# Kernel tuning notes

Hardware: AMD Instinct MI355X
Metric: run time of the kernel (lower is better)

Reference implementation:

```python
import jax, jax.numpy as jnp
import numpy as np

HEAD_DIM = 64
NUM_LANDMARKS = 64
SEQ_LEN = 4096
N_ITER = 6


def setup_inputs() -> dict:
    key = jax.random.key(0)
    kq, kk, kv = jax.random.split(key, 3)
    shape = (4, 12, SEQ_LEN, HEAD_DIM)  # [B, H, S, D]
    return {
        "Q": jax.random.normal(kq, shape, dtype=jnp.float32),
        "K": jax.random.normal(kk, shape, dtype=jnp.float32),
        "V": jax.random.normal(kv, shape, dtype=jnp.float32),
    }


def iterative_inv(mat, n_iter=N_ITER):
    # Newton-Schulz iteration for Moore-Penrose pseudo-inverse.
    L = mat.shape[-1]
    I = jnp.eye(L, dtype=mat.dtype)
    Km = mat
    # global (over all batch/head) max of row/col L1 norms
    scale = 1.0 / (jnp.max(jnp.sum(jnp.abs(Km), axis=-2)) * jnp.max(jnp.sum(jnp.abs(Km), axis=-1)))
    Vm = scale * jnp.swapaxes(Km, -1, -2)
    for _ in range(n_iter):
        KV = jnp.matmul(Km, Vm)
        Vm = jnp.matmul(0.25 * Vm, 13.0 * I - jnp.matmul(KV, 15.0 * I - jnp.matmul(KV, 7.0 * I - KV)))
    return Vm


def reference(Q, K, V):
    B, H, S, D = Q.shape
    m = NUM_LANDMARKS
    inv_scale = 1.0 / np.sqrt(np.sqrt(HEAD_DIM))
    Q = Q * inv_scale
    K = K * inv_scale
    # landmark pooling: mean over segments of length S // m
    Q_land = Q.reshape(B, H, m, S // m, D).mean(axis=-2)  # [B,H,m,D]
    K_land = K.reshape(B, H, m, S // m, D).mean(axis=-2)  # [B,H,m,D]
    kernel_1 = jax.nn.softmax(jnp.einsum("bhsd,bhmd->bhsm", Q, K_land), axis=-1)      # [B,H,S,m]
    kernel_2 = jax.nn.softmax(jnp.einsum("bhmd,bhnd->bhmn", Q_land, K_land), axis=-1)  # [B,H,m,m]
    kernel_3 = jax.nn.softmax(jnp.einsum("bhmd,bhsd->bhms", Q_land, K), axis=-1)       # [B,H,m,S]
    X = jnp.matmul(jnp.matmul(kernel_1, iterative_inv(kernel_2)), jnp.matmul(kernel_3, V))
    return X
```

## Files before the change

### kernel.cpp

```cpp
#include <hip/hip_runtime.h>
#include <cstdint>

#define BH 48
#define SEQ 4096
#define DIM 64
#define SEG 64
#define NCHUNK 8
#define CHUNK 512
#define PAD 68
#define BSTR 72

static constexpr float INV_SCALE = 0.35355339059327379f;

#define OFF_QL   0u
#define OFF_KL   196608u
#define OFF_K2   393216u
#define OFF_W    589824u
#define OFF_P    786432u
#define OFF_MNUM 983040u
#define OFF_MDEN 2555904u
#define OFF_CMAX 2580480u
#define OFF_RMAX 2580528u

typedef __attribute__((ext_vector_type(8))) short short8;
typedef __attribute__((ext_vector_type(4))) float f32x4;
#define MFMA16(a,b,c) __builtin_amdgcn_mfma_f32_16x16x32_bf16(a,b,c,0,0,0)

__device__ __forceinline__ float4 ld4(const float* p){ return *reinterpret_cast<const float4*>(p); }
__device__ __forceinline__ void st4(float* p, float4 v){ *reinterpret_cast<float4*>(p) = v; }

__device__ __forceinline__ unsigned short bfh_(float x){
  unsigned u = __float_as_uint(x);
  return (unsigned short)((u + 0x7fffu + ((u>>16)&1u)) >> 16);
}
__device__ __forceinline__ unsigned short bfl_(float x, unsigned short h){
  float r = x - __uint_as_float(((unsigned)h)<<16);
  return (unsigned short)(__float_as_uint(r) >> 16);
}
__device__ __forceinline__ void split4(float4 v, uint2& hi, uint2& lo){
  unsigned short h0=bfh_(v.x), h1=bfh_(v.y), h2=bfh_(v.z), h3=bfh_(v.w);
  unsigned short l0=bfl_(v.x,h0), l1=bfl_(v.y,h1), l2=bfl_(v.z,h2), l3=bfl_(v.w,h3);
  hi = make_uint2((unsigned)h0 | ((unsigned)h1<<16), (unsigned)h2 | ((unsigned)h3<<16));
  lo = make_uint2((unsigned)l0 | ((unsigned)l1<<16), (unsigned)l2 | ((unsigned)l3<<16));
}
__device__ __forceinline__ short8 mk8(uint2 a, uint2 b){
  union { short8 s; uint4 u; } x; x.u = make_uint4(a.x,a.y,b.x,b.y); return x.s;
}

__device__ __forceinline__ void mm_tile(float c[4][4], const float (*A)[PAD], const float (*B)[PAD], int i0, int j0){
  #pragma unroll 4
  for(int k=0;k<64;k+=4){
    float4 a4[4];
    #pragma unroll
    for(int r=0;r<4;r++) a4[r] = ld4(&A[i0+r][k]);
    #pragma unroll
    for(int kk=0;kk<4;kk++){
      float4 bv = ld4(&B[k+kk][j0]);
      #pragma unroll
      for(int r=0;r<4;r++){
        float a = ((const float*)&a4[r])[kk];
        c[r][0] += a*bv.x; c[r][1] += a*bv.y; c[r][2] += a*bv.z; c[r][3] += a*bv.w;
      }
    }
  }
}

__device__ __forceinline__ void mm_tile_gA(float c[4][4], const float* __restrict__ gA, const float (*B)[PAD], int i0, int j0){
  #pragma unroll 4
  for(int k=0;k<64;k+=4){
    float4 a4[4];
    #pragma unroll
    for(int r=0;r<4;r++) a4[r] = ld4(gA + (i0+r)*64 + k);
    #pragma unroll
    for(int kk=0;kk<4;kk++){
      float4 bv = ld4(&B[k+kk][j0]);
      #pragma unroll
      for(int r=0;r<4;r++){
        float a = ((const float*)&a4[r])[kk];
        c[r][0] += a*bv.x; c[r][1] += a*bv.y; c[r][2] += a*bv.z; c[r][3] += a*bv.w;
      }
    }
  }
}

__device__ __forceinline__ void mm_tile_diag(float c[4][4], const float (*A)[PAD], const float (*B)[PAD], int i0, int j0, float dg){
  #pragma unroll 4
  for(int k=0;k<64;k+=4){
    float4 a4[4];
    #pragma unroll
    for(int r=0;r<4;r++) a4[r] = ld4(&A[i0+r][k]);
    #pragma unroll
    for(int kk=0;kk<4;kk++){
      float4 bv = ld4(&B[k+kk][j0]);
      float b0=-bv.x, b1=-bv.y, b2=-bv.z, b3=-bv.w;
      int dd = k+kk-j0;
      if(dd==0) b0+=dg; else if(dd==1) b1+=dg; else if(dd==2) b2+=dg; else if(dd==3) b3+=dg;
      #pragma unroll
      for(int r=0;r<4;r++){
        float a = ((const float*)&a4[r])[kk];
        c[r][0]+=a*b0; c[r][1]+=a*b1; c[r][2]+=a*b2; c[r][3]+=a*b3;
      }
    }
  }
}

__global__ __launch_bounds__(256) void pool_kernel(const float* __restrict__ Qg, const float* __restrict__ Kg, float* __restrict__ ws){
  int bx = blockIdx.x;
  int head = bx >> 5;
  int rest = bx & 31;
  int tensor = rest >> 4;
  int l0 = (rest & 15) * 4;
  int t = threadIdx.x;
  int ll = t >> 6;
  int lane = t & 63;
  int d4 = (lane & 15) * 4;
  int rq = lane >> 4;
  const float* src = tensor ? Kg : Qg;
  float* dst = ws + (tensor ? OFF_KL : OFF_QL);
  int l = l0 + ll;
  const float* base = src + ((size_t)head*SEQ + (size_t)l*SEG)*DIM + d4;
  float sx=0.f, sy=0.f, sz=0.f, sw=0.f;
  #pragma unroll 4
  for(int r=rq; r<SEG; r+=4){
    float4 v = ld4(base + (size_t)r*DIM);
    sx+=v.x; sy+=v.y; sz+=v.z; sw+=v.w;
  }
  sx += __shfl_xor(sx,16); sy += __shfl_xor(sy,16); sz += __shfl_xor(sz,16); sw += __shfl_xor(sw,16);
  sx += __shfl_xor(sx,32); sy += __shfl_xor(sy,32); sz += __shfl_xor(sz,32); sw += __shfl_xor(sw,32);
  if(rq==0){
    const float sc = INV_SCALE / 64.0f;
    float4 o; o.x=sx*sc; o.y=sy*sc; o.z=sz*sc; o.w=sw*sc;
    st4(dst + ((size_t)head*64 + l)*DIM + d4, o);
  }
}

__global__ __launch_bounds__(256) void k2_kernel(float* __restrict__ ws){
  __shared__ float sQ[64][65];
  __shared__ float sK[64][65];
  __shared__ float sE[64][65];
  __shared__ float red[128];
  int h = blockIdx.x, t = threadIdx.x;
  const float* QL = ws + OFF_QL + (size_t)h*4096;
  const float* KL = ws + OFF_KL + (size_t)h*4096;
  for(int i=t;i<4096;i+=256){ sQ[i>>6][i&63]=QL[i]; sK[i>>6][i&63]=KL[i]; }
  __syncthreads();
  int i = t>>2, q = t&3;
  float l[16];
  #pragma unroll
  for(int jj=0;jj<16;jj++){
    int j = q*16+jj;
    float s=0.f;
    for(int d=0;d<64;d++) s += sQ[i][d]*sK[j][d];
    l[jj]=s;
  }
  float mx = l[0];
  #pragma unroll
  for(int jj=1;jj<16;jj++) mx = fmaxf(mx,l[jj]);
  mx = fmaxf(mx, __shfl_xor(mx,1));
  mx = fmaxf(mx, __shfl_xor(mx,2));
  float sum=0.f;
  #pragma unroll
  for(int jj=0;jj<16;jj++){ l[jj]=__expf(l[jj]-mx); sum+=l[jj]; }
  sum += __shfl_xor(sum,1);
  sum += __shfl_xor(sum,2);
  float inv = 1.0f/sum;
  #pragma unroll
  for(int jj=0;jj<16;jj++) sE[i][q*16+jj] = l[jj]*inv;
  __syncthreads();
  float* K2 = ws + OFF_K2 + (size_t)h*4096;
  for(int idx=t; idx<4096; idx+=256) K2[idx] = sE[idx>>6][idx&63];
  if(t<64){
    float cs=0.f, rs=0.f;
    for(int r=0;r<64;r++){ cs += sE[r][t]; rs += sE[t][r]; }
    red[t]=cs; red[64+t]=rs;
  }
  __syncthreads();
  if(t==0){
    float cm=0.f, rm=0.f;
    for(int j=0;j<64;j++){ cm=fmaxf(cm,red[j]); rm=fmaxf(rm,red[64+j]); }
    ws[OFF_CMAX+h]=cm; ws[OFF_RMAX+h]=rm;
  }
}

__global__ __launch_bounds__(256) void fused_kernel(const float* __restrict__ Kg, const float* __restrict__ Vg, float* __restrict__ ws){
  __shared__ __align__(16) unsigned char smem[74752];
  __shared__ float sscale;
  int bid = blockIdx.x, t = threadIdx.x;
  const int lane=t&63, w=t>>6, ln=lane&15, g=lane>>4;
  const int rr=t>>4, c4=(t&15)*4;
  if(bid < BH){
    int h = bid;
    const float* K2 = ws + OFF_K2 + (size_t)h*4096;
    unsigned short* Uh=(unsigned short*)smem;
    unsigned short* Ul=Uh+4608;
    unsigned short* Rh=Uh+9216;
    unsigned short* Rl=Uh+13824;
    unsigned short* Ch=Uh+18432;
    unsigned short* Cl=Uh+23040;
    unsigned short* Gh=Uh+27648;
    unsigned short* Gl=Uh+32256;
    short8 kmh[2],kml[2];
    #pragma unroll
    for(int kh=0;kh<2;kh++){
      const float* p=K2+(16*w+ln)*64+32*kh+8*g;
      float4 x0=ld4(p), x1=ld4(p+4);
      uint2 h0,l0,h1,l1; split4(x0,h0,l0); split4(x1,h1,l1);
      kmh[kh]=mk8(h0,h1); kml[kh]=mk8(l0,l1);
    }
    if(t<64){
      float cm=(lane<BH)?ws[OFF_CMAX+lane]:0.f;
      float rm=(lane<BH)?ws[OFF_RMAX+lane]:0.f;
      #pragma unroll
      for(int s=32;s>=1;s>>=1){ cm=fmaxf(cm,__shfl_xor(cm,s)); rm=fmaxf(rm,__shfl_xor(rm,s)); }
      if(t==0) sscale=1.0f/(cm*rm);
    }
    __syncthreads();
    float scale=sscale;
    #pragma unroll
    for(int gg=0;gg<4;gg++){
      int m=rr+16*gg;
      float4 v=ld4(K2+m*64+c4);
      v.x*=scale; v.y*=scale; v.z*=scale; v.w*=scale;
      uint2 hi,lo; split4(v,hi,lo);
      *reinterpret_cast<uint2*>(Uh+m*BSTR+c4)=hi;
      *reinterpret_cast<uint2*>(Ul+m*BSTR+c4)=lo;
      float fv[4]={v.x,v.y,v.z,v.w};
      #pragma unroll
      for(int e=0;e<4;e++){
        unsigned short hv=bfh_(fv[e]);
        Rh[(c4+e)*BSTR+m]=hv;
        Rl[(c4+e)*BSTR+m]=bfl_(fv[e],hv);
      }
    }
    __syncthreads();
    f32x4 dA[4];
    short8 ah[2],al[2];
    for(int it=0; it<5; it++){
      #pragma unroll
      for(int ni=0;ni<4;ni++){
        f32x4 d=(f32x4){0.f,0.f,0.f,0.f};
        #pragma unroll
        for(int kh=0;kh<2;kh++){
          int bb=(16*ni+ln)*BSTR+32*kh+8*g;
          short8 bh=*reinterpret_cast<const short8*>(Uh+bb);
          short8 bl=*reinterpret_cast<const short8*>(Ul+bb);
          d=MFMA16(kmh[kh],bh,d); d=MFMA16(kmh[kh],bl,d); d=MFMA16(kml[kh],bh,d);
        }
        dA[ni]=d;
      }
      #pragma unroll
      for(int ni=0;ni<4;ni++){
        int j=16*ni+ln;
        float4 tv; float* pv=(float*)&tv;
        #pragma unroll
        for(int r=0;r<4;r++){
          float v=dA[ni][r];
          int i=16*w+4*g+r;
          unsigned short hv=bfh_(v);
          Ch[i*BSTR+j]=hv; Cl[i*BSTR+j]=bfl_(v,hv);
          pv[r]=((i==j)?7.0f:0.0f)-v;
        }
        uint2 hi,lo; split4(tv,hi,lo);
        *reinterpret_cast<uint2*>(Gh+j*BSTR+16*w+4*g)=hi;
        *reinterpret_cast<uint2*>(Gl+j*BSTR+16*w+4*g)=lo;
      }
      __syncthreads();
      #pragma unroll
      for(int kh=0;kh<2;kh++){
        int ab=(16*w+ln)*BSTR+32*kh+8*g;
        ah[kh]=*reinterpret_cast<const short8*>(Ch+ab);
        al[kh]=*reinterpret_cast<const short8*>(Cl+ab);
      }
      #pragma unroll
      for(int ni=0;ni<4;ni++){
        f32x4 d=(f32x4){0.f,0.f,0.f,0.f};
        #pragma unroll
        for(int kh=0;kh<2;kh++){
          int bb=(16*ni+ln)*BSTR+32*kh+8*g;
          short8 bh=*reinterpret_cast<const short8*>(Gh+bb);
          short8 bl=*reinterpret_cast<const short8*>(Gl+bb);
          d=MFMA16(ah[kh],bh,d); d=MFMA16(ah[kh],bl,d); d=MFMA16(al[kh],bh,d);
        }
        dA[ni]=d;
      }
      __syncthreads();
      #pragma unroll
      for(int ni=0;ni<4;ni++){
        int j=16*ni+ln;
        float4 tv; float* pv=(float*)&tv;
        #pragma unroll
        for(int r=0;r<4;r++){ int i=16*w+4*g+r; pv[r]=((i==j)?15.0f:0.0f)-dA[ni][r]; }
        uint2 hi,lo; split4(tv,hi,lo);
        *reinterpret_cast<uint2*>(Gh+j*BSTR+16*w+4*g)=hi;
        *reinterpret_cast<uint2*>(Gl+j*BSTR+16*w+4*g)=lo;
      }
      __syncthreads();
      #pragma unroll
      for(int ni=0;ni<4;ni++){
        f32x4 d=(f32x4){0.f,0.f,0.f,0.f};
        #pragma unroll
        for(int kh=0;kh<2;kh++){
          int bb=(16*ni+ln)*BSTR+32*kh+8*g;
          short8 bh=*reinterpret_cast<const short8*>(Gh+bb);
          short8 bl=*reinterpret_cast<const short8*>(Gl+bb);
          d=MFMA16(ah[kh],bh,d); d=MFMA16(ah[kh],bl,d); d=MFMA16(al[kh],bh,d);
        }
        dA[ni]=d;
      }
      __syncthreads();
      #pragma unroll
      for(int ni=0;ni<4;ni++){
        int j=16*ni+ln;
        float4 tv; float* pv=(float*)&tv;
        #pragma unroll
        for(int r=0;r<4;r++){ int i=16*w+4*g+r; pv[r]=((i==j)?13.0f:0.0f)-dA[ni][r]; }
        uint2 hi,lo; split4(tv,hi,lo);
        *reinterpret_cast<uint2*>(Ch+j*BSTR+16*w+4*g)=hi;
        *reinterpret_cast<uint2*>(Cl+j*BSTR+16*w+4*g)=lo;
      }
      __syncthreads();
      #pragma unroll
      for(int kh=0;kh<2;kh++){
        int ab=(16*w+ln)*BSTR+32*kh+8*g;
        ah[kh]=*reinterpret_cast<const short8*>(Rh+ab);
        al[kh]=*reinterpret_cast<const short8*>(Rl+ab);
      }
      #pragma unroll
      for(int ni=0;ni<4;ni++){
        f32x4 d=(f32x4){0.f,0.f,0.f,0.f};
        #pragma unroll
        for(int kh=0;kh<2;kh++){
          int bb=(16*ni+ln)*BSTR+32*kh+8*g;
          short8 bh=*reinterpret_cast<const short8*>(Ch+bb);
          short8 bl=*reinterpret_cast<const short8*>(Cl+bb);
          d=MFMA16(ah[kh],bh,d); d=MFMA16(ah[kh],bl,d); d=MFMA16(al[kh],bh,d);
        }
        dA[ni]=d;
      }
      __syncthreads();
      #pragma unroll
      for(int ni=0;ni<4;ni++){
        int j=16*ni+ln;
        float4 tv; float* pv=(float*)&tv;
        #pragma unroll
        for(int r=0;r<4;r++){
          float v=0.25f*dA[ni][r];
          int i=16*w+4*g+r;
          unsigned short hv=bfh_(v);
          Rh[i*BSTR+j]=hv; Rl[i*BSTR+j]=bfl_(v,hv);
          pv[r]=v;
        }
        uint2 hi,lo; split4(tv,hi,lo);
        *reinterpret_cast<uint2*>(Uh+j*BSTR+16*w+4*g)=hi;
        *reinterpret_cast<uint2*>(Ul+j*BSTR+16*w+4*g)=lo;
      }
      __syncthreads();
    }
    float (*Vmf)[PAD]=(float(*)[PAD])(smem+36864);
    for(int i=t;i<4096;i+=256){
      int r_=i>>6, c_=i&63;
      float v=__uint_as_float(((unsigned)Rh[r_*BSTR+c_])<<16)
             +__uint_as_float(((unsigned)Rl[r_*BSTR+c_])<<16);
      Vmf[r_][c_]=v;
    }
    __syncthreads();
    float (*B1)[PAD]=(float(*)[PAD])(smem);
    float (*B2)[PAD]=(float(*)[PAD])(smem+17408);
    int i0=(t>>4)*4, j0=(t&15)*4;
    {
      float c[4][4]={};
      mm_tile_gA(c,K2,Vmf,i0,j0);
      #pragma unroll
      for(int r=0;r<4;r++){ float4 o; o.x=c[r][0];o.y=c[r][1];o.z=c[r][2];o.w=c[r][3]; st4(&B1[i0+r][j0],o); }
      __syncthreads();
    }
    {
      float c[4][4]={};
      mm_tile_diag(c,B1,B1,i0,j0,7.0f);
      #pragma unroll
      for(int r=0;r<4;r++){ float4 o; o.x=c[r][0];o.y=c[r][1];o.z=c[r][2];o.w=c[r][3]; st4(&B2[i0+r][j0],o); }
      __syncthreads();
    }
    {
      float c[4][4]={};
      mm_tile_diag(c,B1,B2,i0,j0,15.0f);
      __syncthreads();
      #pragma unroll
      for(int r=0;r<4;r++){ float4 o; o.x=c[r][0];o.y=c[r][1];o.z=c[r][2];o.w=c[r][3]; st4(&B1[i0+r][j0],o); }
      __syncthreads();
    }
    {
      float c[4][4]={};
      mm_tile_diag(c,Vmf,B1,i0,j0,13.0f);
      __syncthreads();
      #pragma unroll
      for(int r=0;r<4;r++){ float4 o; o.x=0.25f*c[r][0];o.y=0.25f*c[r][1];o.z=0.25f*c[r][2];o.w=0.25f*c[r][3]; st4(&Vmf[i0+r][j0],o); }
      __syncthreads();
    }
    float* W = ws + OFF_W + (size_t)h*4096;
    for(int i=t;i<4096;i+=256) W[i] = Vmf[i>>6][i&63];
  } else {
    int b = bid - BH;
    int h = b >> 3, ch = b & 7;
    unsigned short* QLh=(unsigned short*)smem;
    unsigned short* QLl=QLh+4608;
    unsigned short* Kth=QLh+9216;
    unsigned short* Ktl=QLh+13824;
    unsigned short* VTh=QLh+18432;
    unsigned short* VTl=QLh+23040;
    unsigned short* PTh=QLh+27648;
    unsigned short* PTl=QLh+32256;
    float* sden=(float*)(smem+73728);
    const float* QL = ws + OFF_QL + (size_t)h*4096;
    #pragma unroll
    for(int gg=0;gg<4;gg++){
      int m=rr+16*gg;
      float4 v=ld4(QL+m*64+c4);
      uint2 hi,lo; split4(v,hi,lo);
      *reinterpret_cast<uint2*>(QLh+m*BSTR+c4)=hi;
      *reinterpret_cast<uint2*>(QLl+m*BSTR+c4)=lo;
    }
    const size_t kbase=((size_t)h*SEQ+(size_t)ch*CHUNK)*DIM;
    float4 kr[4],vr[4];
    #pragma unroll
    for(int gg=0;gg<4;gg++){
      size_t off=kbase+(size_t)(rr+16*gg)*DIM+c4;
      kr[gg]=ld4(Kg+off); vr[gg]=ld4(Vg+off);
    }
    f32x4 acc[4];
    #pragma unroll
    for(int ni=0;ni<4;ni++) acc[ni]=(f32x4){0.f,0.f,0.f,0.f};
    float den_acc[4]={0.f,0.f,0.f,0.f};
    for(int tile=0;tile<8;tile++){
      __syncthreads();
      #pragma unroll
      for(int gg=0;gg<4;gg++){
        int r=rr+16*gg;
        float4 kv=kr[gg];
        kv.x*=INV_SCALE; kv.y*=INV_SCALE; kv.z*=INV_SCALE; kv.w*=INV_SCALE;
        uint2 hi,lo; split4(kv,hi,lo);
        *reinterpret_cast<uint2*>(Kth+r*BSTR+c4)=hi;
        *reinterpret_cast<uint2*>(Ktl+r*BSTR+c4)=lo;
        float fv[4]={vr[gg].x,vr[gg].y,vr[gg].z,vr[gg].w};
        #pragma unroll
        for(int e=0;e<4;e++){
          int d=c4+e;
          unsigned short hv=bfh_(fv[e]);
          unsigned short lv=bfl_(fv[e],hv);
          int sp = r ^ (((d>>2)&7)<<3);
          VTh[d*BSTR+sp]=hv; VTl[d*BSTR+sp]=lv;
        }
      }
      if(tile<7){
        #pragma unroll
        for(int gg=0;gg<4;gg++){
          size_t off=kbase+(size_t)((tile+1)*64+rr+16*gg)*DIM+c4;
          kr[gg]=ld4(Kg+off); vr[gg]=ld4(Vg+off);
        }
      }
      __syncthreads();
      short8 kah[2],kal[2];
      #pragma unroll
      for(int kh=0;kh<2;kh++){
        int ab=(16*w+ln)*BSTR+32*kh+8*g;
        kah[kh]=*reinterpret_cast<const short8*>(Kth+ab);
        kal[kh]=*reinterpret_cast<const short8*>(Ktl+ab);
      }
      #pragma unroll
      for(int ni=0;ni<4;ni++){
        f32x4 dl=(f32x4){0.f,0.f,0.f,0.f};
        #pragma unroll
        for(int kh=0;kh<2;kh++){
          int bb=(16*ni+ln)*BSTR+32*kh+8*g;
          short8 bh=*reinterpret_cast<const short8*>(QLh+bb);
          short8 bl=*reinterpret_cast<const short8*>(QLl+bb);
          dl=MFMA16(kah[kh],bh,dl);
          dl=MFMA16(kah[kh],bl,dl);
          dl=MFMA16(kal[kh],bh,dl);
        }
        float p0=__expf(dl[0]), p1=__expf(dl[1]), p2=__expf(dl[2]), p3=__expf(dl[3]);
        den_acc[ni]+=p0+p1+p2+p3;
        unsigned short h0=bfh_(p0),h1=bfh_(p1),h2=bfh_(p2),h3=bfh_(p3);
        unsigned short l0=bfl_(p0,h0),l1=bfl_(p1,h1),l2=bfl_(p2,h2),l3=bfl_(p3,h3);
        int pb=(16*ni+ln)*BSTR+16*w+4*g;
        *reinterpret_cast<uint2*>(PTh+pb)=make_uint2((unsigned)h0|((unsigned)h1<<16),(unsigned)h2|((unsigned)h3<<16));
        *reinterpret_cast<uint2*>(PTl+pb)=make_uint2((unsigned)l0|((unsigned)l1<<16),(unsigned)l2|((unsigned)l3<<16));
      }
      __syncthreads();
      short8 pah[2],pal[2];
      #pragma unroll
      for(int kh=0;kh<2;kh++){
        int pb=(16*w+ln)*BSTR+32*kh+8*g;
        pah[kh]=*reinterpret_cast<const short8*>(PTh+pb);
        pal[kh]=*reinterpret_cast<const short8*>(PTl+pb);
      }
      #pragma unroll
      for(int ni=0;ni<4;ni++){
        int row=16*ni+ln;
        int swz=((row>>2)&7)<<3;
        #pragma unroll
        for(int kh=0;kh<2;kh++){
          int vb=row*BSTR+((32*kh+8*g)^swz);
          short8 vh=*reinterpret_cast<const short8*>(VTh+vb);
          short8 vl=*reinterpret_cast<const short8*>(VTl+vb);
          acc[ni]=MFMA16(pah[kh],vh,acc[ni]);
          acc[ni]=MFMA16(pah[kh],vl,acc[ni]);
          acc[ni]=MFMA16(pal[kh],vh,acc[ni]);
        }
      }
    }
    float* num = ws + OFF_MNUM + (size_t)b*4096;
    #pragma unroll
    for(int ni=0;ni<4;ni++){
      #pragma unroll
      for(int r=0;r<4;r++) num[(16*w+4*g+r)*64+16*ni+ln]=acc[ni][r];
      den_acc[ni]+=__shfl_xor(den_acc[ni],16);
      den_acc[ni]+=__shfl_xor(den_acc[ni],32);
    }
    if(lane<16){
      #pragma unroll
      for(int ni=0;ni<4;ni++) sden[w*64+16*ni+lane]=den_acc[ni];
    }
    __syncthreads();
    if(t<64) ws[OFF_MDEN+(size_t)b*64+t]=sden[t]+sden[64+t]+sden[128+t]+sden[192+t];
  }
}

__global__ __launch_bounds__(256) void combine_kernel(float* __restrict__ ws){
  __shared__ float sW[64][PAD];
  __shared__ float sM[64][PAD];
  __shared__ float sden[64];
  int h=blockIdx.x, t=threadIdx.x;
  if(t<64){
    float s=0.f;
    for(int c=0;c<NCHUNK;c++) s += ws[OFF_MDEN + ((size_t)h*NCHUNK+c)*64 + t];
    sden[t]=1.0f/s;
  }
  for(int i=t;i<4096;i+=256) sW[i>>6][i&63] = ws[OFF_W + (size_t)h*4096 + i];
  __syncthreads();
  for(int i=t;i<1024;i+=256){
    int m=i>>4, d4=(i&15)*4;
    float sx=0.f,sy=0.f,sz=0.f,sw2=0.f;
    for(int c=0;c<NCHUNK;c++){
      float4 v = ld4(ws + OFF_MNUM + ((size_t)h*NCHUNK+c)*4096 + m*64 + d4);
      sx+=v.x; sy+=v.y; sz+=v.z; sw2+=v.w;
    }
    float iv = sden[m];
    float4 o; o.x=sx*iv; o.y=sy*iv; o.z=sz*iv; o.w=sw2*iv;
    st4(&sM[m][d4], o);
  }
  __syncthreads();
  int i0=(t>>4)*4, j0=(t&15)*4;
  float c[4][4]={};
  mm_tile(c, sW, sM, i0, j0);
  float* P = ws + OFF_P + (size_t)h*4096;
  #pragma unroll
  for(int r=0;r<4;r++){
    float4 o; o.x=c[r][0]; o.y=c[r][1]; o.z=c[r][2]; o.w=c[r][3];
    st4(P + (i0+r)*64 + j0, o);
  }
}

__global__ __launch_bounds__(256) void final_kernel(const float* __restrict__ Qg, float* __restrict__ out, const float* __restrict__ ws){
  __shared__ __align__(16) unsigned char smem[37888];
  int bid=blockIdx.x, t=threadIdx.x;
  int h=bid>>6, s0=(bid&63)*64;
  const int lane=t&63, w=t>>6, ln=lane&15, g=lane>>4;
  const int rr=t>>4, c4=(t&15)*4;
  unsigned short* QBh=(unsigned short*)smem;
  unsigned short* QBl=QBh+4608;
  unsigned short* KLh=QBh+9216;
  unsigned short* KLl=QBh+13824;
  float* sdenw=(float*)(smem+36864);
  const float* KL = ws + OFF_KL + (size_t)h*4096;
  const float* P  = ws + OFF_P  + (size_t)h*4096;
  const float* Qb = Qg + ((size_t)h*SEQ + (size_t)s0)*DIM;
  float4 p2r[4];
  #pragma unroll
  for(int gg=0;gg<4;gg++){
    int row=rr+16*gg;
    p2r[gg]=ld4(P+row*64+c4);
    float4 q=ld4(Qb+(size_t)row*DIM+c4);
    q.x*=INV_SCALE; q.y*=INV_SCALE; q.z*=INV_SCALE; q.w*=INV_SCALE;
    uint2 hi,lo; split4(q,hi,lo);
    *reinterpret_cast<uint2*>(QBh+row*BSTR+c4)=hi;
    *reinterpret_cast<uint2*>(QBl+row*BSTR+c4)=lo;
    float4 kl=ld4(KL+row*64+c4);
    split4(kl,hi,lo);
    *reinterpret_cast<uint2*>(KLh+row*BSTR+c4)=hi;
    *reinterpret_cast<uint2*>(KLl+row*BSTR+c4)=lo;
  }
  __syncthreads();
  short8 ah_[2],al_[2];
  #pragma unroll
  for(int kh=0;kh<2;kh++){
    int ab=(16*w+ln)*BSTR+32*kh+8*g;
    ah_[kh]=*reinterpret_cast<const short8*>(KLh+ab);
    al_[kh]=*reinterpret_cast<const short8*>(KLl+ab);
  }
  f32x4 dl[4];
  #pragma unroll
  for(int ni=0;ni<4;ni++){
    f32x4 d=(f32x4){0.f,0.f,0.f,0.f};
    #pragma unroll
    for(int kh=0;kh<2;kh++){
      int bb=(16*ni+ln)*BSTR+32*kh+8*g;
      short8 bh=*reinterpret_cast<const short8*>(QBh+bb);
      short8 bl=*reinterpret_cast<const short8*>(QBl+bb);
      d=MFMA16(ah_[kh],bh,d); d=MFMA16(ah_[kh],bl,d); d=MFMA16(al_[kh],bh,d);
    }
    dl[ni]=d;
  }
  __syncthreads();
  #pragma unroll
  for(int gg=0;gg<4;gg++){
    int row=rr+16*gg;
    float fp[4]={p2r[gg].x,p2r[gg].y,p2r[gg].z,p2r[gg].w};
    #pragma unroll
    for(int e=0;e<4;e++){
      unsigned short hv=bfh_(fp[e]);
      QBh[(c4+e)*BSTR+row]=hv;
      QBl[(c4+e)*BSTR+row]=bfl_(fp[e],hv);
    }
  }
  float den_acc[4];
  #pragma unroll
  for(int ni=0;ni<4;ni++){
    float p0=__expf(dl[ni][0]), p1=__expf(dl[ni][1]), p2v=__expf(dl[ni][2]), p3v=__expf(dl[ni][3]);
    den_acc[ni]=p0+p1+p2v+p3v;
    unsigned short h0=bfh_(p0),h1=bfh_(p1),h2=bfh_(p2v),h3=bfh_(p3v);
    unsigned short e0=bfl_(p0,h0),e1=bfl_(p1,h1),e2=bfl_(p2v,h2),e3=bfl_(p3v,h3);
    int pb=(16*ni+ln)*BSTR+16*w+4*g;
    *reinterpret_cast<uint2*>(KLh+pb)=make_uint2((unsigned)h0|((unsigned)h1<<16),(unsigned)h2|((unsigned)h3<<16));
    *reinterpret_cast<uint2*>(KLl+pb)=make_uint2((unsigned)e0|((unsigned)e1<<16),(unsigned)e2|((unsigned)e3<<16));
    den_acc[ni]+=__shfl_xor(den_acc[ni],16);
    den_acc[ni]+=__shfl_xor(den_acc[ni],32);
  }
  if(lane<16){
    #pragma unroll
    for(int ni=0;ni<4;ni++) sdenw[w*64+16*ni+lane]=den_acc[ni];
  }
  __syncthreads();
  #pragma unroll
  for(int kh=0;kh<2;kh++){
    int ab=(16*w+ln)*BSTR+32*kh+8*g;
    ah_[kh]=*reinterpret_cast<const short8*>(KLh+ab);
    al_[kh]=*reinterpret_cast<const short8*>(KLl+ab);
  }
  float inv[4];
  #pragma unroll
  for(int r=0;r<4;r++){
    int s=16*w+4*g+r;
    inv[r]=1.0f/(sdenw[s]+sdenw[64+s]+sdenw[128+s]+sdenw[192+s]);
  }
  #pragma unroll
  for(int ni=0;ni<4;ni++){
    f32x4 d=(f32x4){0.f,0.f,0.f,0.f};
    #pragma unroll
    for(int kh=0;kh<2;kh++){
      int bb=(16*ni+ln)*BSTR+32*kh+8*g;
      short8 bh=*reinterpret_cast<const short8*>(QBh+bb);
      short8 bl=*reinterpret_cast<const short8*>(QBl+bb);
      d=MFMA16(ah_[kh],bh,d); d=MFMA16(ah_[kh],bl,d); d=MFMA16(al_[kh],bh,d);
    }
    #pragma unroll
    for(int r=0;r<4;r++)
      out[((size_t)h*SEQ + (size_t)(s0+16*w+4*g+r))*DIM + 16*ni+ln] = d[r]*inv[r];
  }
}

extern "C" void kernel_launch(void* const* d_in, const int* in_sizes, int n_in,
                              void* d_out, int out_size, void* d_ws, size_t ws_size,
                              hipStream_t stream) {
  const float* Q = (const float*)d_in[0];
  const float* K = (const float*)d_in[1];
  const float* V = (const float*)d_in[2];
  float* out = (float*)d_out;
  float* ws  = (float*)d_ws;

  pool_kernel   <<<BH*32, 256, 0, stream>>>(Q, K, ws);
  k2_kernel     <<<BH,    256, 0, stream>>>(ws);
  fused_kernel  <<<BH + BH*NCHUNK, 256, 0, stream>>>(K, V, ws);
  combine_kernel<<<BH,    256, 0, stream>>>(ws);
  final_kernel  <<<BH*64, 256, 0, stream>>>(Q, out, ws);
}
```

Baseline: 244.1 us.

## Split sequence into 16 chunks and vectorize V transpose stores

Doubles the number of sequence chunks per head so the kernel_3·V phase launches twice as many blocks, each processing 256 rows. It also changes how V is loaded so each thread holds four consecutive rows of one column group, letting the transposed bf16 hi/lo tiles be written with packed 8-byte stores instead of scalar swizzled stores, and removes the swizzle on reads. The trade-off is a larger partial-result workspace and a heavier final reduction over chunks, plus possible LDS bank conflicts on the unswizzled layout.

```diff
diff --git a/kernel.cpp b/kernel.cpp
--- a/kernel.cpp
+++ b/kernel.cpp
@@ -5,8 +5,8 @@
 #define SEQ 4096
 #define DIM 64
 #define SEG 64
-#define NCHUNK 8
-#define CHUNK 512
+#define NCHUNK 16
+#define CHUNK 256
 #define PAD 68
 #define BSTR 72
 
@@ -18,9 +18,9 @@
 #define OFF_W    589824u
 #define OFF_P    786432u
 #define OFF_MNUM 983040u
-#define OFF_MDEN 2555904u
-#define OFF_CMAX 2580480u
-#define OFF_RMAX 2580528u
+#define OFF_MDEN 4128768u
+#define OFF_CMAX 4177920u
+#define OFF_RMAX 4177968u
 
 typedef __attribute__((ext_vector_type(8))) short short8;
 typedef __attribute__((ext_vector_type(4))) float f32x4;
@@ -401,7 +401,7 @@
     for(int i=t;i<4096;i+=256) W[i] = Vmf[i>>6][i&63];
   } else {
     int b = bid - BH;
-    int h = b >> 3, ch = b & 7;
+    int h = b >> 4, ch = b & 15;
     unsigned short* QLh=(unsigned short*)smem;
     unsigned short* QLl=QLh+4608;
     unsigned short* Kth=QLh+9216;
@@ -411,6 +411,7 @@
     unsigned short* PTh=QLh+27648;
     unsigned short* PTl=QLh+32256;
     float* sden=(float*)(smem+73728);
+    const int va=t&15, vb=t>>4;
     const float* QL = ws + OFF_QL + (size_t)h*4096;
     #pragma unroll
     for(int gg=0;gg<4;gg++){
@@ -424,14 +425,14 @@
     float4 kr[4],vr[4];
     #pragma unroll
     for(int gg=0;gg<4;gg++){
-      size_t off=kbase+(size_t)(rr+16*gg)*DIM+c4;
-      kr[gg]=ld4(Kg+off); vr[gg]=ld4(Vg+off);
+      kr[gg]=ld4(Kg+kbase+(size_t)(rr+16*gg)*DIM+c4);
+      vr[gg]=ld4(Vg+kbase+(size_t)(4*va+gg)*DIM+4*vb);
     }
     f32x4 acc[4];
     #pragma unroll
     for(int ni=0;ni<4;ni++) acc[ni]=(f32x4){0.f,0.f,0.f,0.f};
     float den_acc[4]={0.f,0.f,0.f,0.f};
-    for(int tile=0;tile<8;tile++){
+    for(int tile=0;tile<CHUNK/64;tile++){
       __syncthreads();
       #pragma unroll
       for(int gg=0;gg<4;gg++){
@@ -441,21 +442,22 @@
         uint2 hi,lo; split4(kv,hi,lo);
         *reinterpret_cast<uint2*>(Kth+r*BSTR+c4)=hi;
         *reinterpret_cast<uint2*>(Ktl+r*BSTR+c4)=lo;
-        float fv[4]={vr[gg].x,vr[gg].y,vr[gg].z,vr[gg].w};
-        #pragma unroll
-        for(int e=0;e<4;e++){
-          int d=c4+e;
-          unsigned short hv=bfh_(fv[e]);
-          unsigned short lv=bfl_(fv[e],hv);
-          int sp = r ^ (((d>>2)&7)<<3);
-          VTh[d*BSTR+sp]=hv; VTl[d*BSTR+sp]=lv;
-        }
-      }
-      if(tile<7){
+      }
+      #pragma unroll
+      for(int j=0;j<4;j++){
+        float e0=((const float*)&vr[0])[j], e1=((const float*)&vr[1])[j];
+        float e2=((const float*)&vr[2])[j], e3=((const float*)&vr[3])[j];
+        unsigned short h0=bfh_(e0),h1=bfh_(e1),h2=bfh_(e2),h3=bfh_(e3);
+        unsigned short l0=bfl_(e0,h0),l1=bfl_(e1,h1),l2=bfl_(e2,h2),l3=bfl_(e3,h3);
+        int vo=(4*vb+j)*BSTR+4*va;
+        *reinterpret_cast<uint2*>(VTh+vo)=make_uint2((unsigned)h0|((unsigned)h1<<16),(unsigned)h2|((unsigned)h3<<16));
+        *reinterpret_cast<uint2*>(VTl+vo)=make_uint2((unsigned)l0|((unsigned)l1<<16),(unsigned)l2|((unsigned)l3<<16));
+      }
+      if(tile<CHUNK/64-1){
         #pragma unroll
         for(int gg=0;gg<4;gg++){
-          size_t off=kbase+(size_t)((tile+1)*64+rr+16*gg)*DIM+c4;
-          kr[gg]=ld4(Kg+off); vr[gg]=ld4(Vg+off);
+          kr[gg]=ld4(Kg+kbase+(size_t)((tile+1)*64+rr+16*gg)*DIM+c4);
+          vr[gg]=ld4(Vg+kbase+(size_t)((tile+1)*64+4*va+gg)*DIM+4*vb);
         }
       }
       __syncthreads();
@@ -497,12 +499,11 @@
       #pragma unroll
       for(int ni=0;ni<4;ni++){
         int row=16*ni+ln;
-        int swz=((row>>2)&7)<<3;
         #pragma unroll
         for(int kh=0;kh<2;kh++){
-          int vb=row*BSTR+((32*kh+8*g)^swz);
-          short8 vh=*reinterpret_cast<const short8*>(VTh+vb);
-          short8 vl=*reinterpret_cast<const short8*>(VTl+vb);
+          int vo=row*BSTR+32*kh+8*g;
+          short8 vh=*reinterpret_cast<const short8*>(VTh+vo);
+          short8 vl=*reinterpret_cast<const short8*>(VTl+vo);
           acc[ni]=MFMA16(pah[kh],vh,acc[ni]);
           acc[ni]=MFMA16(pah[kh],vl,acc[ni]);
           acc[ni]=MFMA16(pal[kh],vh,acc[ni]);
```

Result: no change. 241.9 us (-0.9%).
